# Performance work log

Hardware: AMD Instinct MI355X
Metric: run time of the kernel (lower is better)

## Reference

```python
import jax, jax.numpy as jnp
import numpy as np
import math

B, S, H, NH = 1, 2048, 1024, 16  # batch, seq, hidden, heads


def setup_inputs() -> dict:
    key = jax.random.key(0)
    ks = jax.random.split(key, 12)
    inp = {
        "query": jax.random.normal(ks[0], (B, S, H), dtype=jnp.float32),
        "key": jax.random.normal(ks[1], (B, S, H), dtype=jnp.float32),
        "value": jax.random.normal(ks[2], (B, S, H), dtype=jnp.float32),
        "attention_mask": jax.random.randint(ks[3], (1, 1, S, S), 0, 2, dtype=jnp.int32),
        # torch nn.Linear params: y = x @ W.T + b, W init ~ U(-1/sqrt(H), 1/sqrt(H))
        "Wq": jax.random.uniform(ks[4], (H, H), jnp.float32, -1, 1) / math.sqrt(H),
        "bq": jax.random.uniform(ks[5], (H,), jnp.float32, -1, 1) / math.sqrt(H),
        "Wk": jax.random.uniform(ks[6], (H, H), jnp.float32, -1, 1) / math.sqrt(H),
        "bk": jax.random.uniform(ks[7], (H,), jnp.float32, -1, 1) / math.sqrt(H),
        "Wv": jax.random.uniform(ks[8], (H, H), jnp.float32, -1, 1) / math.sqrt(H),
        "bv": jax.random.uniform(ks[9], (H,), jnp.float32, -1, 1) / math.sqrt(H),
        "Wo": jax.random.uniform(ks[10], (H, H), jnp.float32, -1, 1) / math.sqrt(H),
        "bo": jax.random.uniform(ks[11], (H,), jnp.float32, -1, 1) / math.sqrt(H),
        "head": NH,
        "hidden_size": H,
    }
    return inp


def reference(query, key, value, attention_mask, Wq, bq, Wk, bk, Wv, bv, Wo, bo, head, hidden_size):
    b, s, _ = query.shape
    d_k = hidden_size // head

    def proj(x, W, bias):
        # [b, s, hidden] -> [b, head, s, d_k]
        y = x @ W.T + bias
        return y.reshape(b, s, head, d_k).transpose(0, 2, 1, 3)

    q = proj(query, Wq, bq)
    k = proj(key, Wk, bk)
    v = proj(value, Wv, bv)

    # naive full score matrix, as in the source (scale by sqrt(d_k) = last dim of q)
    scores = jnp.einsum("bhqd,bhkd->bhqk", q, k) / math.sqrt(d_k)
    # faithful quirk: masked positions are set to 0 (not -inf) before softmax
    scores = jnp.where(attention_mask == 0, jnp.zeros((), scores.dtype), scores)
    attn = jax.nn.softmax(scores, axis=-1)

    out = jnp.einsum("bhqk,bhkd->bhqd", attn, v)  # [b, head, s, d_k]
    out = out.transpose(0, 2, 1, 3).reshape(b, s, head * d_k)
    return out @ Wo.T + bo
```

## Files before the change

### kernel.cpp

```cpp
#include <hip/hip_runtime.h>
#include <hip/hip_bf16.h>


#define S_LEN 2048
#define HID   1024
#define NHEAD 16
#define DK    64

typedef unsigned short u16;
typedef __attribute__((ext_vector_type(8))) short bf16x8;
typedef __attribute__((ext_vector_type(4))) short bf16x4;
typedef __attribute__((ext_vector_type(4))) float f32x4;

__device__ __forceinline__ void load16_lds(const void* g, void* l) {
  __builtin_amdgcn_global_load_lds(
      (const __attribute__((address_space(1))) void*)g,
      (__attribute__((address_space(3))) void*)l, 16, 0, 0);
}

__device__ __forceinline__ short bfbits(float x) {
  __hip_bfloat16 h = __float2bfloat16(x);
  return *(short*)&h;
}
__device__ __forceinline__ bf16x8 cvt8(float4 a, float4 b) {
  bf16x8 r;
  r[0] = bfbits(a.x); r[1] = bfbits(a.y); r[2] = bfbits(a.z); r[3] = bfbits(a.w);
  r[4] = bfbits(b.x); r[5] = bfbits(b.y); r[6] = bfbits(b.z); r[7] = bfbits(b.w);
  return r;
}
__device__ __forceinline__ float bf2f(u16 u) {
  unsigned v = (unsigned)u << 16;
  return *(float*)&v;
}

__global__ __launch_bounds__(256) void cvtW_kernel(
    const float* __restrict__ wq, const float* __restrict__ wk,
    const float* __restrict__ wv, const float* __restrict__ wo,
    u16* __restrict__ Wbf) {
  const int y = blockIdx.y;
  const float* src = y == 0 ? wq : (y == 1 ? wk : (y == 2 ? wv : wo));
  size_t i = ((size_t)blockIdx.x * 256 + threadIdx.x) * 8;
  float4 a = *(const float4*)(src + i);
  float4 b = *(const float4*)(src + i + 4);
  *(bf16x8*)(Wbf + (size_t)y * (HID * HID) + i) = cvt8(a, b);
}

__global__ void pack_mask_kernel(const int* __restrict__ mask,
                                 unsigned int* __restrict__ bits) {
  int w = blockIdx.x * blockDim.x + threadIdx.x;
  const int4* p = (const int4*)(mask + (size_t)w * 32);
  unsigned word = 0;
#pragma unroll
  for (int i = 0; i < 8; ++i) {
    int4 v = p[i];
    word |= (unsigned)(v.x != 0) << (i * 4 + 0);
    word |= (unsigned)(v.y != 0) << (i * 4 + 1);
    word |= (unsigned)(v.z != 0) << (i * 4 + 2);
    word |= (unsigned)(v.w != 0) << (i * 4 + 3);
  }
  bits[w] = word;
}

__global__ __launch_bounds__(256) void gemm_qkv(
    const float* __restrict__ qf32, const float* __restrict__ kf32,
    const float* __restrict__ vf32, const u16* __restrict__ Wbf,
    const float* __restrict__ bq, const float* __restrict__ bk,
    const float* __restrict__ bv, u16* __restrict__ Qb,
    u16* __restrict__ Kb, u16* __restrict__ Vt) {
  constexpr int Mm = 2048, Nn = 1024, Kk = 1024, NIT = 16;
  const int z = blockIdx.z;
  const float* A = z == 0 ? qf32 : (z == 1 ? kf32 : vf32);
  const u16* W = Wbf + (size_t)z * (HID * HID);
  const float* bias = z == 0 ? bq : (z == 1 ? bk : bv);
  u16* C = z == 0 ? Qb : (z == 1 ? Kb : Vt);
  const float oscale = (z == 0) ? 0.125f * 1.4426950408889634f : 1.0f;
  const int transpose = (z == 2);

  const int tid = threadIdx.x, lane = tid & 63, wave = tid >> 6;
  const int q4 = lane >> 4, c16 = lane & 15;
  const int bx = blockIdx.x;
  const int mBase = (bx & 31) * 64;
  const int nBase = (bx >> 5) * 128;
  const int wn = wave * 32;

  __shared__ __align__(16) u16 As[2][2][64 * 32];
  __shared__ __align__(16) u16 Bs[2][2][128 * 32];

  f32x4 acc[4][2] = {};
  const int srow = lane >> 2, se8 = (lane & 3) * 8;

  auto issueW = [&](int it, int buf) {
#pragma unroll
    for (int j = 0; j < 4; ++j) {
      int u = wave * 4 + j, h = u >> 3, grp = u & 7;
      load16_lds(W + (size_t)(nBase + grp * 16 + srow) * Kk + it * 64 +
                     h * 32 + se8,
                 &Bs[buf][h][grp * 512]);
    }
  };
  float4 ar[2][2];
  auto loadA = [&](int it) {
#pragma unroll
    for (int j = 0; j < 2; ++j) {
      int u = wave * 2 + j, h = u >> 2, grp = u & 3;
      const float* s = A + (size_t)(mBase + grp * 16 + srow) * Kk + it * 64 +
                       h * 32 + se8;
      ar[j][0] = *(const float4*)s;
      ar[j][1] = *(const float4*)(s + 4);
    }
  };
  auto storeA = [&](int buf) {
#pragma unroll
    for (int j = 0; j < 2; ++j) {
      int u = wave * 2 + j, h = u >> 2, grp = u & 3;
      *(bf16x8*)&As[buf][h][grp * 512 + srow * 32 + se8] =
          cvt8(ar[j][0], ar[j][1]);
    }
  };

  loadA(0);
  storeA(0);
  issueW(0, 0);
  __syncthreads();

  for (int it = 0; it < NIT; ++it) {
    const int buf = it & 1, nbuf = buf ^ 1;
    if (it + 1 < NIT) {
      issueW(it + 1, nbuf);
      loadA(it + 1);
    }
#pragma unroll
    for (int kk = 0; kk < 2; ++kk) {
      bf16x8 af[4], bfr[2];
#pragma unroll
      for (int t = 0; t < 4; ++t)
        af[t] = *(const bf16x8*)&As[buf][kk][(t * 16 + c16) * 32 + q4 * 8];
#pragma unroll
      for (int t = 0; t < 2; ++t)
        bfr[t] = *(const bf16x8*)&Bs[buf][kk][(wn + t * 16 + c16) * 32 + q4 * 8];
#pragma unroll
      for (int mt = 0; mt < 4; ++mt)
#pragma unroll
        for (int nt = 0; nt < 2; ++nt)
          acc[mt][nt] = __builtin_amdgcn_mfma_f32_16x16x32_bf16(
              af[mt], bfr[nt], acc[mt][nt], 0, 0, 0);
    }
    if (it + 1 < NIT) storeA(nbuf);
    __syncthreads();
  }

#pragma unroll
  for (int nt = 0; nt < 2; ++nt) {
    int col = nBase + wn + nt * 16 + c16;
    float bv2 = bias[col];
#pragma unroll
    for (int mt = 0; mt < 4; ++mt) {
#pragma unroll
      for (int r = 0; r < 4; ++r) {
        int row = mBase + mt * 16 + q4 * 4 + r;
        float v = (acc[mt][nt][r] + bv2) * oscale;
        if (transpose)
          ((__hip_bfloat16*)C)[(size_t)col * Mm + row] = __float2bfloat16(v);
        else
          ((__hip_bfloat16*)C)[(size_t)row * Nn + col] = __float2bfloat16(v);
      }
    }
  }
}

__global__ __launch_bounds__(256) void attn_kernel(
    const u16* __restrict__ Qb, const u16* __restrict__ Kb,
    const u16* __restrict__ Vt, const unsigned* __restrict__ mbits,
    u16* __restrict__ partO, float* __restrict__ partL) {
  constexpr int NITA = S_LEN / 2 / 64;
  const int qt = blockIdx.x, h = blockIdx.y, zz = blockIdx.z;
  const int tid = threadIdx.x, lane = tid & 63, wave = tid >> 6;
  const int q4 = lane >> 4, c16 = lane & 15;

  __shared__ __align__(16) u16 Ks[2][2][64 * 32];
  __shared__ __align__(16) u16 Vs[2][2][64 * 32];
  __shared__ __align__(16) u16 Ps[4][16 * 72];

  const int wq0 = qt * 64 + wave * 16;

  bf16x8 qf[2];
#pragma unroll
  for (int kk = 0; kk < 2; ++kk)
    qf[kk] = *(const bf16x8*)(Qb + (size_t)(wq0 + c16) * HID + h * DK +
                              kk * 32 + q4 * 8);

  f32x4 o[4] = {};
  float l_lane[4] = {};

  const int srow = lane >> 2;
  const int se8  = (lane & 3) * 8;
  const int kvbase = zz * (S_LEN / 2);

  auto issueKV = [&](int it, int buf) {
    const int kv0 = kvbase + it * 64;
#pragma unroll
    for (int j = 0; j < 4; ++j) {
      int i = wave * 4 + j;
      if (i < 8) {
        int half = i >> 2, grp = i & 3;
        load16_lds(Kb + (size_t)(kv0 + grp * 16 + srow) * HID + h * DK +
                       half * 32 + se8,
                   &Ks[buf][half][grp * 512]);
      } else {
        int ii = i - 8;
        int half = ii >> 2, grp = ii & 3;
        load16_lds(Vt + (size_t)(h * DK + grp * 16 + srow) * S_LEN + kv0 +
                       half * 32 + se8,
                   &Vs[buf][half][grp * 512]);
      }
    }
  };

  issueKV(0, 0);
  __syncthreads();

  for (int it = 0; it < NITA; ++it) {
    const int buf = it & 1, nbuf = buf ^ 1;
    const int kv0 = kvbase + it * 64;
    if (it + 1 < NITA) issueKV(it + 1, nbuf);

    f32x4 sv[4];
#pragma unroll
    for (int nt = 0; nt < 4; ++nt) {
      bf16x8 kf0 = *(const bf16x8*)&Ks[buf][0][(nt * 16 + c16) * 32 + q4 * 8];
      bf16x8 kf1 = *(const bf16x8*)&Ks[buf][1][(nt * 16 + c16) * 32 + q4 * 8];
      f32x4 a = {};
      a = __builtin_amdgcn_mfma_f32_16x16x32_bf16(qf[0], kf0, a, 0, 0, 0);
      a = __builtin_amdgcn_mfma_f32_16x16x32_bf16(qf[1], kf1, a, 0, 0, 0);
      sv[nt] = a;
    }

#pragma unroll
    for (int r = 0; r < 4; ++r) {
      int row = wq0 + q4 * 4 + r;
      const unsigned* mrow = mbits + (size_t)row * 64 + (kv0 >> 5);
      unsigned w0 = mrow[0], w1 = mrow[1];
#pragma unroll
      for (int nt = 0; nt < 4; ++nt) {
        unsigned word = (nt < 2) ? w0 : w1;
        int bit = ((nt & 1) * 16) + c16;
        float s = ((word >> bit) & 1u) ? sv[nt][r] : 0.0f;
        float p = exp2f(s);
        sv[nt][r] = p;
        l_lane[r] += p;
      }
    }

    u16* pw = &Ps[wave][0];
#pragma unroll
    for (int r = 0; r < 4; ++r)
#pragma unroll
      for (int nt = 0; nt < 4; ++nt)
        ((__hip_bfloat16*)pw)[(q4 * 4 + r) * 72 + nt * 16 + c16] =
            __float2bfloat16(sv[nt][r]);
    asm volatile("s_waitcnt lgkmcnt(0)" ::: "memory");

#pragma unroll
    for (int kk = 0; kk < 2; ++kk) {
      bf16x8 pa = *(const bf16x8*)&pw[c16 * 72 + kk * 32 + q4 * 8];
#pragma unroll
      for (int nt = 0; nt < 4; ++nt) {
        bf16x8 vb = *(const bf16x8*)&Vs[buf][kk][(nt * 16 + c16) * 32 + q4 * 8];
        o[nt] = __builtin_amdgcn_mfma_f32_16x16x32_bf16(pa, vb, o[nt], 0, 0, 0);
      }
    }
    __syncthreads();
  }

#pragma unroll
  for (int r = 0; r < 4; ++r) {
    float s = l_lane[r];
#pragma unroll
    for (int d = 1; d < 16; d <<= 1) s += __shfl_xor(s, d);
    l_lane[r] = s;
  }

#pragma unroll
  for (int r = 0; r < 4; ++r) {
    int row = wq0 + q4 * 4 + r;
#pragma unroll
    for (int nt = 0; nt < 4; ++nt)
      ((__hip_bfloat16*)partO)[((size_t)zz * S_LEN + row) * HID + h * DK +
                               nt * 16 + c16] = __float2bfloat16(o[nt][r]);
    if (c16 == 0)
      partL[((size_t)zz * NHEAD + h) * S_LEN + row] = l_lane[r];
  }
}

__global__ __launch_bounds__(256) void combine_kernel(
    const u16* __restrict__ partO, const float* __restrict__ partL,
    u16* __restrict__ ctx) {
  size_t idx = ((size_t)blockIdx.x * 256 + threadIdx.x) * 4;
  int row = (int)(idx >> 10);
  int col = (int)(idx & 1023);
  int h = col >> 6;
  float l = partL[(size_t)h * S_LEN + row] +
            partL[((size_t)NHEAD + h) * S_LEN + row];
  float inv = 1.0f / l;
  bf16x4 a = *(const bf16x4*)(partO + idx);
  bf16x4 b = *(const bf16x4*)(partO + (size_t)S_LEN * HID + idx);
  bf16x4 r;
#pragma unroll
  for (int j = 0; j < 4; ++j) {
    float v = (bf2f((u16)a[j]) + bf2f((u16)b[j])) * inv;
    r[j] = bfbits(v);
  }
  *(bf16x4*)(ctx + idx) = r;
}

__global__ __launch_bounds__(256) void gemm_out(
    const u16* __restrict__ ctx, const u16* __restrict__ Wo,
    const float* __restrict__ bo, float* __restrict__ out) {
  constexpr int Nn = 1024, Kk = 1024, NIT = 16;
  const int tid = threadIdx.x, lane = tid & 63, wave = tid >> 6;
  const int q4 = lane >> 4, c16 = lane & 15;
  const int bx = blockIdx.x;
  const int mBase = (bx & 63) * 32;
  const int nBase = (bx >> 6) * 128;
  const int wn = wave * 32;

  __shared__ __align__(16) u16 As[2][2][32 * 32];
  __shared__ __align__(16) u16 Bs[2][2][128 * 32];

  f32x4 acc[2][2] = {};
  const int srow = lane >> 2, se8 = (lane & 3) * 8;

  auto issue = [&](int it, int buf) {
    {
      int u = wave, h = u >> 1, grp = u & 1;
      load16_lds(ctx + (size_t)(mBase + grp * 16 + srow) * Kk + it * 64 +
                     h * 32 + se8,
                 &As[buf][h][grp * 512]);
    }
#pragma unroll
    for (int j = 0; j < 4; ++j) {
      int u = wave * 4 + j, h = u >> 3, grp = u & 7;
      load16_lds(Wo + (size_t)(nBase + grp * 16 + srow) * Kk + it * 64 +
                     h * 32 + se8,
                 &Bs[buf][h][grp * 512]);
    }
  };

  issue(0, 0);
  __syncthreads();

  for (int it = 0; it < NIT; ++it) {
    const int buf = it & 1, nbuf = buf ^ 1;
    if (it + 1 < NIT) issue(it + 1, nbuf);
#pragma unroll
    for (int kk = 0; kk < 2; ++kk) {
      bf16x8 af[2], bfr[2];
#pragma unroll
      for (int t = 0; t < 2; ++t)
        af[t] = *(const bf16x8*)&As[buf][kk][(t * 16 + c16) * 32 + q4 * 8];
#pragma unroll
      for (int t = 0; t < 2; ++t)
        bfr[t] = *(const bf16x8*)&Bs[buf][kk][(wn + t * 16 + c16) * 32 + q4 * 8];
#pragma unroll
      for (int mt = 0; mt < 2; ++mt)
#pragma unroll
        for (int nt = 0; nt < 2; ++nt)
          acc[mt][nt] = __builtin_amdgcn_mfma_f32_16x16x32_bf16(
              af[mt], bfr[nt], acc[mt][nt], 0, 0, 0);
    }
    __syncthreads();
  }

#pragma unroll
  for (int nt = 0; nt < 2; ++nt) {
    int col = nBase + wn + nt * 16 + c16;
    float bv = bo[col];
#pragma unroll
    for (int mt = 0; mt < 2; ++mt)
#pragma unroll
      for (int r = 0; r < 4; ++r) {
        int row = mBase + mt * 16 + q4 * 4 + r;
        out[(size_t)row * Nn + col] = acc[mt][nt][r] + bv;
      }
  }
}

extern "C" void kernel_launch(void* const* d_in, const int* in_sizes, int n_in,
                              void* d_out, int out_size, void* d_ws, size_t ws_size,
                              hipStream_t stream) {
  const float* q    = (const float*)d_in[0];
  const float* k    = (const float*)d_in[1];
  const float* v    = (const float*)d_in[2];
  const int*   mask = (const int*)d_in[3];
  const float* Wq = (const float*)d_in[4];
  const float* bq = (const float*)d_in[5];
  const float* Wk = (const float*)d_in[6];
  const float* bk = (const float*)d_in[7];
  const float* Wv = (const float*)d_in[8];
  const float* bv = (const float*)d_in[9];
  const float* Wo = (const float*)d_in[10];
  const float* bo = (const float*)d_in[11];

  const size_t M2 = (size_t)S_LEN * HID;
  const size_t W1 = (size_t)HID * HID;
  const size_t need = (4 * W1 + 2 * M2 + 3 * M2) * 2 +
                      (size_t)S_LEN * 64 * 4 + 2 * NHEAD * S_LEN * 4;
  if (ws_size < need) return;

  u16* Wbf = (u16*)d_ws;
  u16* partO = Wbf + 4 * W1;
  u16* Qb = partO + 2 * M2;
  u16* Kb = Qb + M2;
  u16* Vt = Kb + M2;
  unsigned* mbits = (unsigned*)(Vt + M2);
  float* partL = (float*)(mbits + (size_t)S_LEN * 64);
  u16* ctx = Qb;

  hipLaunchKernelGGL(cvtW_kernel, dim3(512, 4), dim3(256), 0, stream,
                     Wq, Wk, Wv, Wo, Wbf);

  hipLaunchKernelGGL(pack_mask_kernel, dim3((S_LEN * (S_LEN / 32)) / 256),
                     dim3(256), 0, stream, mask, mbits);

  hipLaunchKernelGGL(gemm_qkv, dim3(256, 1, 3), dim3(256), 0, stream,
                     q, k, v, Wbf, bq, bk, bv, Qb, Kb, Vt);

  hipLaunchKernelGGL(attn_kernel, dim3(S_LEN / 64, NHEAD, 2), dim3(256), 0,
                     stream, Qb, Kb, Vt, mbits, partO, partL);

  hipLaunchKernelGGL(combine_kernel, dim3((S_LEN * HID / 4) / 256), dim3(256),
                     0, stream, partO, partL, ctx);

  hipLaunchKernelGGL(gemm_out, dim3(512), dim3(256), 0, stream,
                     ctx, Wbf + 3 * W1, bo, (float*)d_out);
}
```

Baseline: 213.4 us.

## Fuse split-KV combine into output GEMM and double query rows per attention wave

Removes the separate combine kernel: the output GEMM now loads both partial attention outputs and the row sums, normalises them in registers, and writes the bf16 A tile into LDS itself. Each attention wave now handles 32 query rows instead of 16, so every K/V tile loaded into LDS is reused twice, at the cost of more registers and half as many blocks. It also switches exp2f to the hardware exp2 builtin. The fused A path gives up the async global-to-LDS load for register loads plus conversion, which may expose latency in the GEMM.

```diff
diff --git a/kernel.cpp b/kernel.cpp
--- a/kernel.cpp
+++ b/kernel.cpp
@@ -9,8 +9,17 @@
 
 typedef unsigned short u16;
 typedef __attribute__((ext_vector_type(8))) short bf16x8;
-typedef __attribute__((ext_vector_type(4))) short bf16x4;
 typedef __attribute__((ext_vector_type(4))) float f32x4;
+
+#if defined(__has_builtin)
+#if __has_builtin(__builtin_amdgcn_exp2f)
+#define EXP2F(x) __builtin_amdgcn_exp2f(x)
+#else
+#define EXP2F(x) exp2f(x)
+#endif
+#else
+#define EXP2F(x) exp2f(x)
+#endif
 
 __device__ __forceinline__ void load16_lds(const void* g, void* l) {
   __builtin_amdgcn_global_load_lds(
@@ -179,18 +188,20 @@
 
   __shared__ __align__(16) u16 Ks[2][2][64 * 32];
   __shared__ __align__(16) u16 Vs[2][2][64 * 32];
-  __shared__ __align__(16) u16 Ps[4][16 * 72];
-
-  const int wq0 = qt * 64 + wave * 16;
-
-  bf16x8 qf[2];
-#pragma unroll
-  for (int kk = 0; kk < 2; ++kk)
-    qf[kk] = *(const bf16x8*)(Qb + (size_t)(wq0 + c16) * HID + h * DK +
-                              kk * 32 + q4 * 8);
-
-  f32x4 o[4] = {};
-  float l_lane[4] = {};
+  __shared__ __align__(16) u16 Ps[4][2 * 16 * 72];
+
+  const int wq0 = qt * 128 + wave * 32;
+
+  bf16x8 qf[2][2];
+#pragma unroll
+  for (int t = 0; t < 2; ++t)
+#pragma unroll
+    for (int kk = 0; kk < 2; ++kk)
+      qf[t][kk] = *(const bf16x8*)(Qb + (size_t)(wq0 + t * 16 + c16) * HID +
+                                   h * DK + kk * 32 + q4 * 8);
+
+  f32x4 o[2][4] = {};
+  float l_lane[2][4] = {};
 
   const int srow = lane >> 2;
   const int se8  = (lane & 3) * 8;
@@ -224,99 +235,99 @@
     const int kv0 = kvbase + it * 64;
     if (it + 1 < NITA) issueKV(it + 1, nbuf);
 
-    f32x4 sv[4];
+    f32x4 sv[2][4];
 #pragma unroll
     for (int nt = 0; nt < 4; ++nt) {
       bf16x8 kf0 = *(const bf16x8*)&Ks[buf][0][(nt * 16 + c16) * 32 + q4 * 8];
       bf16x8 kf1 = *(const bf16x8*)&Ks[buf][1][(nt * 16 + c16) * 32 + q4 * 8];
-      f32x4 a = {};
-      a = __builtin_amdgcn_mfma_f32_16x16x32_bf16(qf[0], kf0, a, 0, 0, 0);
-      a = __builtin_amdgcn_mfma_f32_16x16x32_bf16(qf[1], kf1, a, 0, 0, 0);
-      sv[nt] = a;
-    }
-
+#pragma unroll
+      for (int t = 0; t < 2; ++t) {
+        f32x4 a = {};
+        a = __builtin_amdgcn_mfma_f32_16x16x32_bf16(qf[t][0], kf0, a, 0, 0, 0);
+        a = __builtin_amdgcn_mfma_f32_16x16x32_bf16(qf[t][1], kf1, a, 0, 0, 0);
+        sv[t][nt] = a;
+      }
+    }
+
+#pragma unroll
+    for (int t = 0; t < 2; ++t)
+#pragma unroll
+      for (int r = 0; r < 4; ++r) {
+        int row = wq0 + t * 16 + q4 * 4 + r;
+        const unsigned* mrow = mbits + (size_t)row * 64 + (kv0 >> 5);
+        unsigned w0 = mrow[0], w1 = mrow[1];
+#pragma unroll
+        for (int nt = 0; nt < 4; ++nt) {
+          unsigned word = (nt < 2) ? w0 : w1;
+          int bit = ((nt & 1) * 16) + c16;
+          float s = ((word >> bit) & 1u) ? sv[t][nt][r] : 0.0f;
+          float p = EXP2F(s);
+          sv[t][nt][r] = p;
+          l_lane[t][r] += p;
+        }
+      }
+
+    u16* pw = &Ps[wave][0];
+#pragma unroll
+    for (int t = 0; t < 2; ++t)
+#pragma unroll
+      for (int r = 0; r < 4; ++r)
+#pragma unroll
+        for (int nt = 0; nt < 4; ++nt)
+          ((__hip_bfloat16*)pw)[t * 1152 + (q4 * 4 + r) * 72 + nt * 16 + c16] =
+              __float2bfloat16(sv[t][nt][r]);
+    asm volatile("s_waitcnt lgkmcnt(0)" ::: "memory");
+
+    bf16x8 vb[2][4];
+#pragma unroll
+    for (int kk = 0; kk < 2; ++kk)
+#pragma unroll
+      for (int nt = 0; nt < 4; ++nt)
+        vb[kk][nt] =
+            *(const bf16x8*)&Vs[buf][kk][(nt * 16 + c16) * 32 + q4 * 8];
+#pragma unroll
+    for (int t = 0; t < 2; ++t)
+#pragma unroll
+      for (int kk = 0; kk < 2; ++kk) {
+        bf16x8 pa = *(const bf16x8*)&pw[t * 1152 + c16 * 72 + kk * 32 + q4 * 8];
+#pragma unroll
+        for (int nt = 0; nt < 4; ++nt)
+          o[t][nt] = __builtin_amdgcn_mfma_f32_16x16x32_bf16(pa, vb[kk][nt],
+                                                             o[t][nt], 0, 0, 0);
+      }
+    __syncthreads();
+  }
+
+#pragma unroll
+  for (int t = 0; t < 2; ++t)
 #pragma unroll
     for (int r = 0; r < 4; ++r) {
-      int row = wq0 + q4 * 4 + r;
-      const unsigned* mrow = mbits + (size_t)row * 64 + (kv0 >> 5);
-      unsigned w0 = mrow[0], w1 = mrow[1];
-#pragma unroll
-      for (int nt = 0; nt < 4; ++nt) {
-        unsigned word = (nt < 2) ? w0 : w1;
-        int bit = ((nt & 1) * 16) + c16;
-        float s = ((word >> bit) & 1u) ? sv[nt][r] : 0.0f;
-        float p = exp2f(s);
-        sv[nt][r] = p;
-        l_lane[r] += p;
-      }
-    }
-
-    u16* pw = &Ps[wave][0];
-#pragma unroll
-    for (int r = 0; r < 4; ++r)
+      float s = l_lane[t][r];
+#pragma unroll
+      for (int d = 1; d < 16; d <<= 1) s += __shfl_xor(s, d);
+      l_lane[t][r] = s;
+    }
+
+#pragma unroll
+  for (int t = 0; t < 2; ++t)
+#pragma unroll
+    for (int r = 0; r < 4; ++r) {
+      int row = wq0 + t * 16 + q4 * 4 + r;
 #pragma unroll
       for (int nt = 0; nt < 4; ++nt)
-        ((__hip_bfloat16*)pw)[(q4 * 4 + r) * 72 + nt * 16 + c16] =
-            __float2bfloat16(sv[nt][r]);
-    asm volatile("s_waitcnt lgkmcnt(0)" ::: "memory");
-
-#pragma unroll
-    for (int kk = 0; kk < 2; ++kk) {
-      bf16x8 pa = *(const bf16x8*)&pw[c16 * 72 + kk * 32 + q4 * 8];
-#pragma unroll
-      for (int nt = 0; nt < 4; ++nt) {
-        bf16x8 vb = *(const bf16x8*)&Vs[buf][kk][(nt * 16 + c16) * 32 + q4 * 8];
-        o[nt] = __builtin_amdgcn_mfma_f32_16x16x32_bf16(pa, vb, o[nt], 0, 0, 0);
-      }
-    }
-    __syncthreads();
-  }
-
-#pragma unroll
-  for (int r = 0; r < 4; ++r) {
-    float s = l_lane[r];
-#pragma unroll
-    for (int d = 1; d < 16; d <<= 1) s += __shfl_xor(s, d);
-    l_lane[r] = s;
-  }
-
-#pragma unroll
-  for (int r = 0; r < 4; ++r) {
-    int row = wq0 + q4 * 4 + r;
-#pragma unroll
-    for (int nt = 0; nt < 4; ++nt)
-      ((__hip_bfloat16*)partO)[((size_t)zz * S_LEN + row) * HID + h * DK +
-                               nt * 16 + c16] = __float2bfloat16(o[nt][r]);
-    if (c16 == 0)
-      partL[((size_t)zz * NHEAD + h) * S_LEN + row] = l_lane[r];
-  }
-}
-
-__global__ __launch_bounds__(256) void combine_kernel(
+        ((__hip_bfloat16*)partO)[((size_t)zz * S_LEN + row) * HID + h * DK +
+                                 nt * 16 + c16] = __float2bfloat16(o[t][nt][r]);
+      if (c16 == 0)
+        partL[((size_t)zz * NHEAD + h) * S_LEN + row] = l_lane[t][r];
+    }
+}
+
+__global__ __launch_bounds__(256) void gemm_out(
     const u16* __restrict__ partO, const float* __restrict__ partL,
-    u16* __restrict__ ctx) {
-  size_t idx = ((size_t)blockIdx.x * 256 + threadIdx.x) * 4;
-  int row = (int)(idx >> 10);
-  int col = (int)(idx & 1023);
-  int h = col >> 6;
-  float l = partL[(size_t)h * S_LEN + row] +
-            partL[((size_t)NHEAD + h) * S_LEN + row];
-  float inv = 1.0f / l;
-  bf16x4 a = *(const bf16x4*)(partO + idx);
-  bf16x4 b = *(const bf16x4*)(partO + (size_t)S_LEN * HID + idx);
-  bf16x4 r;
-#pragma unroll
-  for (int j = 0; j < 4; ++j) {
-    float v = (bf2f((u16)a[j]) + bf2f((u16)b[j])) * inv;
-    r[j] = bfbits(v);
-  }
-  *(bf16x4*)(ctx + idx) = r;
-}
-
-__global__ __launch_bounds__(256) void gemm_out(
-    const u16* __restrict__ ctx, const u16* __restrict__ Wo,
-    const float* __restrict__ bo, float* __restrict__ out) {
+    const u16* __restrict__ Wo, const float* __restrict__ bo,
+    float* __restrict__ out) {
   constexpr int Nn = 1024, Kk = 1024, NIT = 16;
+  constexpr size_t M2 = (size_t)S_LEN * HID;
   const int tid = threadIdx.x, lane = tid & 63, wave = tid >> 6;
   const int q4 = lane >> 4, c16 = lane & 15;
   const int bx = blockIdx.x;
@@ -330,13 +341,7 @@
   f32x4 acc[2][2] = {};
   const int srow = lane >> 2, se8 = (lane & 3) * 8;
 
-  auto issue = [&](int it, int buf) {
-    {
-      int u = wave, h = u >> 1, grp = u & 1;
-      load16_lds(ctx + (size_t)(mBase + grp * 16 + srow) * Kk + it * 64 +
-                     h * 32 + se8,
-                 &As[buf][h][grp * 512]);
-    }
+  auto issueW = [&](int it, int buf) {
 #pragma unroll
     for (int j = 0; j < 4; ++j) {
       int u = wave * 4 + j, h = u >> 3, grp = u & 7;
@@ -345,13 +350,38 @@
                  &Bs[buf][h][grp * 512]);
     }
   };
-
-  issue(0, 0);
+  bf16x8 a0r, a1r;
+  float invr;
+  auto loadA = [&](int it) {
+    int u = wave, h = u >> 1, grp = u & 1;
+    int row = mBase + grp * 16 + srow;
+    size_t off = (size_t)row * Kk + it * 64 + h * 32 + se8;
+    a0r = *(const bf16x8*)(partO + off);
+    a1r = *(const bf16x8*)(partO + M2 + off);
+    float l = partL[(size_t)it * S_LEN + row] +
+              partL[((size_t)NHEAD + it) * S_LEN + row];
+    invr = 1.0f / l;
+  };
+  auto storeA = [&](int buf) {
+    int u = wave, h = u >> 1, grp = u & 1;
+    bf16x8 r;
+#pragma unroll
+    for (int j = 0; j < 8; ++j)
+      r[j] = bfbits((bf2f((u16)a0r[j]) + bf2f((u16)a1r[j])) * invr);
+    *(bf16x8*)&As[buf][h][grp * 512 + srow * 32 + se8] = r;
+  };
+
+  loadA(0);
+  storeA(0);
+  issueW(0, 0);
   __syncthreads();
 
   for (int it = 0; it < NIT; ++it) {
     const int buf = it & 1, nbuf = buf ^ 1;
-    if (it + 1 < NIT) issue(it + 1, nbuf);
+    if (it + 1 < NIT) {
+      issueW(it + 1, nbuf);
+      loadA(it + 1);
+    }
 #pragma unroll
     for (int kk = 0; kk < 2; ++kk) {
       bf16x8 af[2], bfr[2];
@@ -368,6 +398,7 @@
           acc[mt][nt] = __builtin_amdgcn_mfma_f32_16x16x32_bf16(
               af[mt], bfr[nt], acc[mt][nt], 0, 0, 0);
     }
+    if (it + 1 < NIT) storeA(nbuf);
     __syncthreads();
   }
 
@@ -414,7 +445,6 @@
   u16* Vt = Kb + M2;
   unsigned* mbits = (unsigned*)(Vt + M2);
   float* partL = (float*)(mbits + (size_t)S_LEN * 64);
-  u16* ctx = Qb;
 
   hipLaunchKernelGGL(cvtW_kernel, dim3(512, 4), dim3(256), 0, stream,
                      Wq, Wk, Wv, Wo, Wbf);
@@ -425,12 +455,9 @@
   hipLaunchKernelGGL(gemm_qkv, dim3(256, 1, 3), dim3(256), 0, stream,
                      q, k, v, Wbf, bq, bk, bv, Qb, Kb, Vt);
 
-  hipLaunchKernelGGL(attn_kernel, dim3(S_LEN / 64, NHEAD, 2), dim3(256), 0,
+  hipLaunchKernelGGL(attn_kernel, dim3(S_LEN / 128, NHEAD, 2), dim3(256), 0,
                      stream, Qb, Kb, Vt, mbits, partO, partL);
 
-  hipLaunchKernelGGL(combine_kernel, dim3((S_LEN * HID / 4) / 256), dim3(256),
-                     0, stream, partO, partL, ctx);
-
   hipLaunchKernelGGL(gemm_out, dim3(512), dim3(256), 0, stream,
-                     ctx, Wbf + 3 * W1, bo, (float*)d_out);
-}
+                     partO, partL, Wbf + 3 * W1, bo, (float*)d_out);
+}
```

New measurement: 206.0 us. 3.5% less time.
